# Kernel optimization log

Hardware: AMD Instinct MI355X
Metric: run time of the kernel (lower is better)

## Reference

```python
import jax, jax.numpy as jnp
import numpy as np

E, T, H, I, K = 16, 2048, 1024, 512, 2  # experts, tokens, hidden, intermediate, top_k


def setup_inputs() -> dict:
    key = jax.random.key(0)
    k1, k2, k3, k4, k5 = jax.random.split(key, 5)
    hidden_states = jax.random.normal(k1, (T, H), dtype=jnp.float32)
    topk_weights = jax.random.uniform(k2, (T, K), dtype=jnp.float32)
    topk_indices = jax.random.randint(k3, (T, K), 0, E, dtype=jnp.int32)
    # learned expert params, viewed per expert as in _view_experts_weight()
    gate_up_proj = jax.random.normal(k4, (E, H, 2 * I), dtype=jnp.float32) * 0.02
    down_proj = jax.random.normal(k5, (E, I, H), dtype=jnp.float32) * 0.02
    return {
        "hidden_states": hidden_states,
        "topk_weights": topk_weights,
        "topk_indices": topk_indices,
        "gate_up_proj": gate_up_proj,
        "down_proj": down_proj,
    }


def reference(hidden_states, topk_weights, topk_indices, gate_up_proj, down_proj):
    """MoE experts: per-expert gate_up GEMM -> silu-gate -> down GEMM,
    combined with top-k routing weights (index_add over tokens in the original).

    Equivalent dense formulation: combine[e, t] = sum_k topk_weights[t, k] * [topk_indices[t, k] == e];
    out = sum_e expert_e(hidden_states) * combine[e][:, None]. Tokens not routed to e get
    weight 0, matching the original gather/scatter-add exactly (including duplicate
    expert ids within a token, which accumulate).
    """
    num_experts = gate_up_proj.shape[0]
    one_hot = jax.nn.one_hot(topk_indices, num_experts, dtype=topk_weights.dtype)  # [T, K, E]
    combine = jnp.einsum("tk,tke->et", topk_weights, one_hot)  # [E, T]

    def body(acc, xs):
        w_gu, w_d, w = xs  # [H, 2I], [I, H], [T]
        gate_up = hidden_states @ w_gu  # [T, 2I]
        gate, up = jnp.split(gate_up, 2, axis=-1)
        expert_out = (jax.nn.silu(gate) * up) @ w_d  # [T, H]
        return acc + expert_out * w[:, None], None

    init = jnp.zeros_like(hidden_states)
    out, _ = jax.lax.scan(body, init, (gate_up_proj, down_proj, combine))
    return out.astype(hidden_states.dtype)
```

## Files before the change

### kernel.cpp

```cpp
#include <hip/hip_runtime.h>

#define E_ 16
#define T_ 2048
#define H_ 1024
#define I_ 512
#define NPAIR 4096
#define BM 128
#define MAXTILE 48

typedef __bf16 bf16x8 __attribute__((ext_vector_type(8)));
typedef float  f32x4  __attribute__((ext_vector_type(4)));

static __device__ __forceinline__ unsigned short f2bf(float f) {
    __bf16 h = (__bf16)f;
    return __builtin_bit_cast(unsigned short, h);
}

static __device__ __forceinline__ uint4 pack8(const float* v) {
    union { unsigned short us[8]; uint4 u; } r;
    #pragma unroll
    for (int i = 0; i < 8; ++i) r.us[i] = f2bf(v[i]);
    return r.u;
}

static __device__ __forceinline__ void gl_lds16(const void* g, void* l) {
    __builtin_amdgcn_global_load_lds(
        (const __attribute__((address_space(1))) unsigned int*)g,
        (__attribute__((address_space(3))) unsigned int*)l,
        16, 0, 0);
}

#define RAW_BARRIER_LGKM                                                \
    asm volatile("s_waitcnt lgkmcnt(0)" ::: "memory");                  \
    asm volatile("s_barrier" ::: "memory");

__global__ __launch_bounds__(256) void route_kernel(
    const float* __restrict__ tw, const int* __restrict__ ti,
    int* __restrict__ offs, int* __restrict__ tile_e, int* __restrict__ tile_r,
    int* __restrict__ pair_ts, float* __restrict__ pair_w, int* __restrict__ inv)
{
    __shared__ unsigned short hist[256][E_];
    __shared__ int ebase[E_];
    const int tid = threadIdx.x;

    int e_loc[16];
    unsigned short h[E_];
    for (int e = 0; e < E_; ++e) h[e] = 0;
    for (int i = 0; i < 16; ++i) {
        int p = tid * 16 + i;
        int e = ti[p];
        e_loc[i] = e;
        h[e]++;
    }
    for (int e = 0; e < E_; ++e) hist[tid][e] = h[e];
    __syncthreads();

    if (tid < E_) {
        int e = tid, run = 0;
        for (int t = 0; t < 256; ++t) {
            unsigned short c = hist[t][e];
            hist[t][e] = (unsigned short)run;
            run += c;
        }
        ebase[e] = run;
    }
    __syncthreads();
    if (tid == 0) {
        int run = 0, nt = 0;
        for (int e = 0; e < E_; ++e) {
            int c = ebase[e];
            offs[e] = run; ebase[e] = run;
            for (int r = 0; r < c; r += BM) { tile_e[nt] = e; tile_r[nt] = r; ++nt; }
            run += c;
        }
        offs[E_] = run;
        for (; nt < MAXTILE; ++nt) tile_e[nt] = -1;
    }
    __syncthreads();

    int cur[E_];
    for (int e = 0; e < E_; ++e) cur[e] = ebase[e] + hist[tid][e];
    for (int i = 0; i < 16; ++i) {
        int p = tid * 16 + i;
        int e = e_loc[i];
        int pos = cur[e]++;
        pair_ts[pos] = p;
        pair_w[pos]  = tw[p];
        inv[p]       = pos;
    }
}

__global__ __launch_bounds__(256) void gather_kernel(
    const float* __restrict__ X, const int* __restrict__ pair_ts,
    unsigned short* __restrict__ Ag)
{
    const int q = blockIdx.x;
    const int t = pair_ts[q] >> 1;
    const int c = threadIdx.x * 4;
    const float4 x = *(const float4*)&X[(size_t)t * H_ + c];
    ushort4 b; b.x = f2bf(x.x); b.y = f2bf(x.y); b.z = f2bf(x.z); b.w = f2bf(x.w);
    *(ushort4*)&Ag[(size_t)q * H_ + c] = b;
}

__global__ __launch_bounds__(256, 4) void transform_kernel(
    const float* __restrict__ W1, const float* __restrict__ W2,
    unsigned short* __restrict__ W1t, unsigned short* __restrict__ W2t)
{
    __shared__ float tile[2][64][65];
    const int t  = threadIdx.x;
    const int c4 = t & 15, r0 = t >> 4;
    const int bid = blockIdx.x;
    float4 r[4];

    if (bid < 1024) {
        const int cb = bid & 15, ksg = (bid >> 4) & 3, e = bid >> 6;
        const float* __restrict__ src = W1 + (size_t)e * (H_ * 2 * I_)
            + ((c4 < 8) ? (cb * 32 + c4 * 4) : (I_ + cb * 32 + (c4 - 8) * 4));
        unsigned short* __restrict__ dstb =
            W1t + ((size_t)(e * 16 + cb) * 16 + ksg * 4) * 4096;
        const int ks0 = ksg * 4;

        #pragma unroll
        for (int i = 0; i < 4; ++i)
            r[i] = *(const float4*)(src + (size_t)(ks0 * 64 + r0 + i * 16) * (2 * I_));
        #pragma unroll
        for (int i = 0; i < 4; ++i) *(float4*)&tile[0][r0 + i * 16][c4 * 4] = r[i];
        RAW_BARRIER_LGKM
        #pragma unroll
        for (int s = 0; s < 4; ++s) {
            if (s + 1 < 4) {
                #pragma unroll
                for (int i = 0; i < 4; ++i)
                    r[i] = *(const float4*)(src + (size_t)((ks0 + s + 1) * 64 + r0 + i * 16) * (2 * I_));
            }
            unsigned short* __restrict__ dst = dstb + s * 4096;
            #pragma unroll
            for (int s2 = 0; s2 < 2; ++s2) {
                int gidx = t * 2 + s2, bn = gidx >> 3, p = gidx & 7;
                int kl = (p ^ (bn & 7)) * 8;
                int c  = ((bn >> 4) & 1) * 32 + (bn >> 5) * 16 + (bn & 15);
                float v[8];
                #pragma unroll
                for (int j = 0; j < 8; ++j) v[j] = tile[s & 1][kl + j][c];
                *(uint4*)&dst[(size_t)gidx * 8] = pack8(v);
            }
            if (s + 1 < 4) {
                #pragma unroll
                for (int i = 0; i < 4; ++i)
                    *(float4*)&tile[(s + 1) & 1][r0 + i * 16][c4 * 4] = r[i];
                RAW_BARRIER_LGKM
            }
        }
    } else {
        const int b2 = bid - 1024;
        const int hb = b2 & 15, ksg = (b2 >> 4) & 1, e = b2 >> 5;
        const float* __restrict__ src = W2 + (size_t)e * (I_ * H_) + hb * 64 + c4 * 4;
        unsigned short* __restrict__ dstb =
            W2t + ((size_t)(e * 16 + hb) * 8 + ksg * 4) * 4096;
        const int ks0 = ksg * 4;

        #pragma unroll
        for (int i = 0; i < 4; ++i)
            r[i] = *(const float4*)(src + (size_t)(ks0 * 64 + r0 + i * 16) * H_);
        #pragma unroll
        for (int i = 0; i < 4; ++i) *(float4*)&tile[0][r0 + i * 16][c4 * 4] = r[i];
        RAW_BARRIER_LGKM
        #pragma unroll
        for (int s = 0; s < 4; ++s) {
            if (s + 1 < 4) {
                #pragma unroll
                for (int i = 0; i < 4; ++i)
                    r[i] = *(const float4*)(src + (size_t)((ks0 + s + 1) * 64 + r0 + i * 16) * H_);
            }
            unsigned short* __restrict__ dst = dstb + s * 4096;
            #pragma unroll
            for (int s2 = 0; s2 < 2; ++s2) {
                int gidx = t * 2 + s2, bn = gidx >> 3, p = gidx & 7;
                int kl = (p ^ (bn & 7)) * 8;
                float v[8];
                #pragma unroll
                for (int j = 0; j < 8; ++j) v[j] = tile[s & 1][kl + j][bn];
                *(uint4*)&dst[(size_t)gidx * 8] = pack8(v);
            }
            if (s + 1 < 4) {
                #pragma unroll
                for (int i = 0; i < 4; ++i)
                    *(float4*)&tile[(s + 1) & 1][r0 + i * 16][c4 * 4] = r[i];
                RAW_BARRIER_LGKM
            }
        }
    }
}

#define MFMA_TILE(AS, BS)                                                              \
    _Pragma("unroll")                                                                  \
    for (int kkj = 0; kkj < 2; ++kkj) {                                                \
        const int j0 = kkj * 4;                                                        \
        bf16x8 af[4], bfr[2];                                                          \
        _Pragma("unroll")                                                              \
        for (int m = 0; m < 4; ++m)                                                    \
            af[m] = *(const bf16x8*)&AS[wm * 64 + m * 16 + lrow][((j0 + lk) ^ (lrow & 7)) * 8]; \
        _Pragma("unroll")                                                              \
        for (int n = 0; n < 2; ++n)                                                    \
            bfr[n] = *(const bf16x8*)&BS[wn * 32 + n * 16 + lrow][((j0 + lk) ^ (lrow & 7)) * 8]; \
        _Pragma("unroll")                                                              \
        for (int m = 0; m < 4; ++m)                                                    \
            _Pragma("unroll")                                                          \
            for (int n = 0; n < 2; ++n)                                                \
                acc[m][n] = __builtin_amdgcn_mfma_f32_16x16x32_bf16(af[m], bfr[n], acc[m][n], 0, 0, 0); \
    }

#define STAGE_A(BUF, KB)                                                               \
    _Pragma("unroll")                                                                  \
    for (int i = 0; i < 4; ++i) gl_lds16(asrc[i] + (KB), &As[BUF][w * 32 + i * 8][0]);

#define STAGE_B(BUF, KS)                                                               \
    _Pragma("unroll")                                                                  \
    for (int i = 0; i < 2; ++i)                                                        \
        gl_lds16(bsrcB + (size_t)(KS) * 4096 + i * 512,                                \
                 &Bs[BUF][0][0] + w * 1024 + i * 512);

#define K_PIPE(NT)                                                                     \
    STAGE_A(0, 0)                                                                      \
    STAGE_B(0, 0)                                                                      \
    __syncthreads();                                                                   \
    int cur = 0;                                                                       \
    _Pragma("unroll")                                                                  \
    for (int kt = 0; kt < (NT); ++kt) {                                                \
        int nxt = cur ^ 1;                                                             \
        if (kt + 1 < (NT)) { STAGE_A(nxt, (kt + 1) * 64) STAGE_B(nxt, kt + 1) }        \
        __builtin_amdgcn_s_setprio(1);                                                 \
        MFMA_TILE(As[cur], Bs[cur])                                                    \
        __builtin_amdgcn_s_setprio(0);                                                 \
        __syncthreads();                                                               \
        cur = nxt;                                                                     \
    }

__global__ __launch_bounds__(256, 3) void gemm1_kernel(
    const unsigned short* __restrict__ Ag, const unsigned short* __restrict__ W1t,
    const int* __restrict__ offs, const int* __restrict__ tile_e,
    const int* __restrict__ tile_r, unsigned short* __restrict__ act)
{
    const int e = tile_e[blockIdx.y];
    if (e < 0) return;
    const int rbeg = offs[e], rend = offs[e + 1];
    const int ne   = rend - rbeg;
    const int row0 = tile_r[blockIdx.y];
    const int cb   = blockIdx.x;
    const int c0   = cb * 32;

    __shared__ unsigned short As[2][128][64];
    __shared__ unsigned short Bs[2][64][64];

    const int tid  = threadIdx.x;
    const int lane = tid & 63;
    const int w    = tid >> 6;
    const int wm   = w >> 1, wn = w & 1;
    const int lrow = lane & 15;
    const int lk   = lane >> 4;

    const int r8 = lane >> 3, gr = lane & 7;
    const unsigned short* asrc[4];
    #pragma unroll
    for (int i = 0; i < 4; ++i) {
        int q = rbeg + row0 + w * 32 + i * 8 + r8;
        if (q > rend - 1) q = rend - 1;
        asrc[i] = Ag + (size_t)q * H_ + (gr ^ r8) * 8;
    }

    const unsigned short* bsrcB =
        W1t + ((size_t)(e * 16 + cb) * 16) * 4096 + w * 1024 + lane * 8;

    f32x4 acc[4][2];
    #pragma unroll
    for (int m = 0; m < 4; ++m)
        #pragma unroll
        for (int n = 0; n < 2; ++n)
            acc[m][n] = f32x4{0.f, 0.f, 0.f, 0.f};

    K_PIPE(16)

    for (int m = 0; m < 4; ++m) {
        #pragma unroll
        for (int reg = 0; reg < 4; ++reg) {
            int rloc = wm * 64 + m * 16 + lk * 4 + reg;
            if (row0 + rloc < ne) {
                int q = rbeg + row0 + rloc;
                float g = acc[m][0][reg], u = acc[m][1][reg];
                float a = g / (1.f + __expf(-g)) * u;
                act[(size_t)q * I_ + c0 + wn * 16 + lrow] = f2bf(a);
            }
        }
    }
}

__global__ __launch_bounds__(256, 3) void gemm2_kernel(
    const unsigned short* __restrict__ Agact, const unsigned short* __restrict__ W2t,
    const int* __restrict__ offs, const int* __restrict__ tile_e,
    const int* __restrict__ tile_r, const float* __restrict__ pair_w,
    float* __restrict__ C2)
{
    const int e = tile_e[blockIdx.y];
    if (e < 0) return;
    const int rbeg = offs[e], rend = offs[e + 1];
    const int ne   = rend - rbeg;
    const int row0 = tile_r[blockIdx.y];
    const int hb   = blockIdx.x;
    const int c0   = hb * 64;

    __shared__ unsigned short As[2][128][64];
    __shared__ unsigned short Bs[2][64][64];

    const int tid  = threadIdx.x;
    const int lane = tid & 63;
    const int w    = tid >> 6;
    const int wm   = w >> 1, wn = w & 1;
    const int lrow = lane & 15;
    const int lk   = lane >> 4;

    const int r8 = lane >> 3, gr = lane & 7;
    const unsigned short* asrc[4];
    #pragma unroll
    for (int i = 0; i < 4; ++i) {
        int q = rbeg + row0 + w * 32 + i * 8 + r8;
        if (q > rend - 1) q = rend - 1;
        asrc[i] = Agact + (size_t)q * I_ + (gr ^ r8) * 8;
    }

    const unsigned short* bsrcB =
        W2t + ((size_t)(e * 16 + hb) * 8) * 4096 + w * 1024 + lane * 8;

    f32x4 acc[4][2];
    #pragma unroll
    for (int m = 0; m < 4; ++m)
        #pragma unroll
        for (int n = 0; n < 2; ++n)
            acc[m][n] = f32x4{0.f, 0.f, 0.f, 0.f};

    K_PIPE(8)

    for (int m = 0; m < 4; ++m) {
        #pragma unroll
        for (int reg = 0; reg < 4; ++reg) {
            int rloc = wm * 64 + m * 16 + lk * 4 + reg;
            if (row0 + rloc < ne) {
                int q   = rbeg + row0 + rloc;
                float wt = pair_w[q];
                #pragma unroll
                for (int n = 0; n < 2; ++n) {
                    int cg = c0 + wn * 32 + n * 16 + lrow;
                    C2[(size_t)q * H_ + cg] = wt * acc[m][n][reg];
                }
            }
        }
    }
}

__global__ __launch_bounds__(256) void combine_kernel(
    const float* __restrict__ C2, const int* __restrict__ inv,
    float* __restrict__ out)
{
    const int t = blockIdx.x;
    const int c = threadIdx.x * 4;
    const int q0 = inv[2 * t], q1 = inv[2 * t + 1];
    const float4 a = *(const float4*)&C2[(size_t)q0 * H_ + c];
    const float4 b = *(const float4*)&C2[(size_t)q1 * H_ + c];
    float4 o;
    o.x = a.x + b.x; o.y = a.y + b.y; o.z = a.z + b.z; o.w = a.w + b.w;
    *(float4*)&out[(size_t)t * H_ + c] = o;
}

extern "C" void kernel_launch(void* const* d_in, const int* in_sizes, int n_in,
                              void* d_out, int out_size, void* d_ws, size_t ws_size,
                              hipStream_t stream)
{
    const float* X  = (const float*)d_in[0];
    const float* tw = (const float*)d_in[1];
    const int*   ti = (const int*)d_in[2];
    const float* W1 = (const float*)d_in[3];
    const float* W2 = (const float*)d_in[4];
    float* out = (float*)d_out;

    char* ws = (char*)d_ws;
    int*   offs    = (int*)(ws);
    int*   tile_e  = (int*)(ws + 128);
    int*   tile_r  = (int*)(ws + 320);
    int*   pair_ts = (int*)(ws + 1024);
    float* pair_w  = (float*)(ws + 1024 + NPAIR * 4);
    int*   inv     = (int*)(ws + 1024 + NPAIR * 8);
    unsigned short* Ag  = (unsigned short*)(ws + (size_t)(1u << 16));
    unsigned short* act = (unsigned short*)(ws + (size_t)(1u << 16) + 8388608);
    unsigned short* W1t = (unsigned short*)(ws + (size_t)(1u << 16) + 12582912);
    unsigned short* W2t = (unsigned short*)(ws + (size_t)(1u << 16) + 46137344);
    float*          C2  = (float*)(ws + (size_t)(1u << 16) + 62914560);

    transform_kernel<<<1536, 256, 0, stream>>>(W1, W2, W1t, W2t);

    route_kernel<<<1, 256, 0, stream>>>(tw, ti, offs, tile_e, tile_r, pair_ts, pair_w, inv);

    gather_kernel<<<NPAIR, 256, 0, stream>>>(X, pair_ts, Ag);

    gemm1_kernel<<<dim3(16, MAXTILE), 256, 0, stream>>>(Ag, W1t, offs, tile_e, tile_r, act);

    gemm2_kernel<<<dim3(16, MAXTILE), 256, 0, stream>>>(act, W2t, offs, tile_e, tile_r, pair_w, C2);

    combine_kernel<<<T_, 256, 0, stream>>>(C2, inv, out);
}
```

Before: 85.87 us.

## Restructure weight transform to wide row loads with bf16 LDS staging

Rewrites the fp32-to-bf16 weight transform kernel so each block reads 64 rows by 512 contiguous columns in four 128-column chunks, converts to bf16 before staging in shared memory, and writes swizzled 16-byte output fragments. The grid is halved to 768 blocks. The intent is more coalesced, wider global reads and half the shared-memory traffic, since tiles hold bf16 instead of fp32. The trade-off is fewer blocks, more registers per thread (16 float4s in flight), and more complex index math for the swizzled output layout.

```diff
diff --git a/kernel.cpp b/kernel.cpp
--- a/kernel.cpp
+++ b/kernel.cpp
@@ -102,94 +102,85 @@
     *(ushort4*)&Ag[(size_t)q * H_ + c] = b;
 }
 
+#define TLOADC(R, CH)                                                                  \
+    _Pragma("unroll")                                                                  \
+    for (int i = 0; i < 8; ++i)                                                        \
+        R[i] = *(const float4*)(src + (size_t)((t >> 5) + i * 8) * 1024 + (CH) * 128 + (t & 31) * 4);
+
+#define TWRC(B, R)                                                                     \
+    _Pragma("unroll")                                                                  \
+    for (int i = 0; i < 8; ++i) {                                                      \
+        ushort4 u_;                                                                    \
+        u_.x = f2bf(R[i].x); u_.y = f2bf(R[i].y); u_.z = f2bf(R[i].z); u_.w = f2bf(R[i].w); \
+        *(ushort4*)&tile[B][(t >> 5) + i * 8][(t & 31) * 4] = u_;                      \
+    }
+
+#define TPACKC(CH, B)                                                                  \
+    {                                                                                  \
+        const int cl = (CH) * 128 + (t >> 1);                                          \
+        int bn_; size_t dstoff;                                                        \
+        if (isW1) {                                                                    \
+            int cb = cl >> 5, grp = (cl >> 4) & 1, sub = cl & 15;                      \
+            bn_ = grp * 32 + half * 16 + sub;                                          \
+            dstoff = ((size_t)((e * 16 + cb) * 16 + ks)) * 4096;                       \
+        } else {                                                                       \
+            int gcol = half * 512 + cl;                                                \
+            int hb = gcol >> 6; bn_ = gcol & 63;                                       \
+            dstoff = ((size_t)((e * 16 + hb) * 8 + ks)) * 4096;                        \
+        }                                                                              \
+        unsigned short* dp = dstO + dstoff + bn_ * 64;                                 \
+        _Pragma("unroll")                                                              \
+        for (int u = 0; u < 4; ++u) {                                                  \
+            int p = (t & 1) * 4 + u;                                                   \
+            int kl = (p ^ (bn_ & 7)) * 8;                                              \
+            union { unsigned short us[8]; uint4 q; } g_;                               \
+            _Pragma("unroll")                                                          \
+            for (int j = 0; j < 8; ++j) g_.us[j] = tile[B][kl + j][t >> 1];            \
+            *(uint4*)&dp[p * 8] = g_.q;                                                \
+        }                                                                              \
+    }
+
 __global__ __launch_bounds__(256, 4) void transform_kernel(
     const float* __restrict__ W1, const float* __restrict__ W2,
     unsigned short* __restrict__ W1t, unsigned short* __restrict__ W2t)
 {
-    __shared__ float tile[2][64][65];
-    const int t  = threadIdx.x;
-    const int c4 = t & 15, r0 = t >> 4;
+    __shared__ unsigned short tile[2][64][140];
+    const int t   = threadIdx.x;
     const int bid = blockIdx.x;
-    float4 r[4];
-
-    if (bid < 1024) {
-        const int cb = bid & 15, ksg = (bid >> 4) & 3, e = bid >> 6;
-        const float* __restrict__ src = W1 + (size_t)e * (H_ * 2 * I_)
-            + ((c4 < 8) ? (cb * 32 + c4 * 4) : (I_ + cb * 32 + (c4 - 8) * 4));
-        unsigned short* __restrict__ dstb =
-            W1t + ((size_t)(e * 16 + cb) * 16 + ksg * 4) * 4096;
-        const int ks0 = ksg * 4;
-
-        #pragma unroll
-        for (int i = 0; i < 4; ++i)
-            r[i] = *(const float4*)(src + (size_t)(ks0 * 64 + r0 + i * 16) * (2 * I_));
-        #pragma unroll
-        for (int i = 0; i < 4; ++i) *(float4*)&tile[0][r0 + i * 16][c4 * 4] = r[i];
-        RAW_BARRIER_LGKM
-        #pragma unroll
-        for (int s = 0; s < 4; ++s) {
-            if (s + 1 < 4) {
-                #pragma unroll
-                for (int i = 0; i < 4; ++i)
-                    r[i] = *(const float4*)(src + (size_t)((ks0 + s + 1) * 64 + r0 + i * 16) * (2 * I_));
-            }
-            unsigned short* __restrict__ dst = dstb + s * 4096;
-            #pragma unroll
-            for (int s2 = 0; s2 < 2; ++s2) {
-                int gidx = t * 2 + s2, bn = gidx >> 3, p = gidx & 7;
-                int kl = (p ^ (bn & 7)) * 8;
-                int c  = ((bn >> 4) & 1) * 32 + (bn >> 5) * 16 + (bn & 15);
-                float v[8];
-                #pragma unroll
-                for (int j = 0; j < 8; ++j) v[j] = tile[s & 1][kl + j][c];
-                *(uint4*)&dst[(size_t)gidx * 8] = pack8(v);
-            }
-            if (s + 1 < 4) {
-                #pragma unroll
-                for (int i = 0; i < 4; ++i)
-                    *(float4*)&tile[(s + 1) & 1][r0 + i * 16][c4 * 4] = r[i];
-                RAW_BARRIER_LGKM
-            }
-        }
+
+    const float* src;
+    unsigned short* dstO;
+    int isW1, half, ks, e;
+    if (bid < 512) {
+        isW1 = 1;
+        half = bid & 1; ks = (bid >> 1) & 15; e = bid >> 5;
+        src  = W1 + (size_t)e * (H_ * 2 * I_) + (size_t)(ks * 64) * (2 * I_) + half * 512;
+        dstO = W1t;
     } else {
-        const int b2 = bid - 1024;
-        const int hb = b2 & 15, ksg = (b2 >> 4) & 1, e = b2 >> 5;
-        const float* __restrict__ src = W2 + (size_t)e * (I_ * H_) + hb * 64 + c4 * 4;
-        unsigned short* __restrict__ dstb =
-            W2t + ((size_t)(e * 16 + hb) * 8 + ksg * 4) * 4096;
-        const int ks0 = ksg * 4;
-
-        #pragma unroll
-        for (int i = 0; i < 4; ++i)
-            r[i] = *(const float4*)(src + (size_t)(ks0 * 64 + r0 + i * 16) * H_);
-        #pragma unroll
-        for (int i = 0; i < 4; ++i) *(float4*)&tile[0][r0 + i * 16][c4 * 4] = r[i];
-        RAW_BARRIER_LGKM
-        #pragma unroll
-        for (int s = 0; s < 4; ++s) {
-            if (s + 1 < 4) {
-                #pragma unroll
-                for (int i = 0; i < 4; ++i)
-                    r[i] = *(const float4*)(src + (size_t)((ks0 + s + 1) * 64 + r0 + i * 16) * H_);
-            }
-            unsigned short* __restrict__ dst = dstb + s * 4096;
-            #pragma unroll
-            for (int s2 = 0; s2 < 2; ++s2) {
-                int gidx = t * 2 + s2, bn = gidx >> 3, p = gidx & 7;
-                int kl = (p ^ (bn & 7)) * 8;
-                float v[8];
-                #pragma unroll
-                for (int j = 0; j < 8; ++j) v[j] = tile[s & 1][kl + j][bn];
-                *(uint4*)&dst[(size_t)gidx * 8] = pack8(v);
-            }
-            if (s + 1 < 4) {
-                #pragma unroll
-                for (int i = 0; i < 4; ++i)
-                    *(float4*)&tile[(s + 1) & 1][r0 + i * 16][c4 * 4] = r[i];
-                RAW_BARRIER_LGKM
-            }
-        }
-    }
+        int b2 = bid - 512;
+        isW1 = 0;
+        half = b2 & 1; ks = (b2 >> 1) & 7; e = b2 >> 4;
+        src  = W2 + (size_t)e * (I_ * H_) + (size_t)(ks * 64) * H_ + half * 512;
+        dstO = W2t;
+    }
+
+    float4 r0[8], r1[8];
+    TLOADC(r0, 0)
+    TWRC(0, r0)
+    TLOADC(r1, 1)
+    RAW_BARRIER_LGKM
+    TPACKC(0, 0)
+    TWRC(1, r1)
+    TLOADC(r0, 2)
+    RAW_BARRIER_LGKM
+    TPACKC(1, 1)
+    TWRC(0, r0)
+    TLOADC(r1, 3)
+    RAW_BARRIER_LGKM
+    TPACKC(2, 0)
+    TWRC(1, r1)
+    RAW_BARRIER_LGKM
+    TPACKC(3, 1)
 }
 
 #define MFMA_TILE(AS, BS)                                                              \
@@ -394,7 +385,7 @@
     unsigned short* W2t = (unsigned short*)(ws + (size_t)(1u << 16) + 46137344);
     float*          C2  = (float*)(ws + (size_t)(1u << 16) + 62914560);
 
-    transform_kernel<<<1536, 256, 0, stream>>>(W1, W2, W1t, W2t);
+    transform_kernel<<<768, 256, 0, stream>>>(W1, W2, W1t, W2t);
 
     route_kernel<<<1, 256, 0, stream>>>(tw, ti, offs, tile_e, tile_r, pair_ts, pair_w, inv);
 
```

Result: slower. 91.55 us (+6.6%).
